# Kernel optimization log

Hardware: AMD Instinct MI355X
Metric: run time of the kernel (lower is better)

Reference implementation:

```python
import jax, jax.numpy as jnp
import numpy as np

PI = 3.141592653589793
M = 1500.0; IZ = 2250.0; LF = 1.2; LR = 1.6; CF = 80000.0; CR = 80000.0
TAU_A = 0.1; TAU_DELTA = 0.1
MAX_STEER = 30.0 * PI / 180.0
MAX_ACCEL = 3.0; MIN_ACCEL = -6.0
MU = 0.9; G = 9.81
L = LF + LR
FY_F_MAX = MU * M * G * (LR / L)
FY_R_MAX = MU * M * G * (LF / L)
V_EFF_MIN = 20.0 / 3.6
DT = 0.1
DT_INT = 0.01
B = 4194304


def setup_inputs() -> dict:
    key = jax.random.key(0)
    k1, k2 = jax.random.split(key)
    init_state = jax.random.normal(k1, (B, 9), dtype=jnp.float32)
    action = jax.random.normal(k2, (B, 2), dtype=jnp.float32)
    return {"init_state": init_state, "action": action}


def _substep(state, a_ref, h):
    # state: (B, 9) = [x, y, psi, v, a, delta, beta, r, delta_ref]
    x, y, psi, v, a, delta, beta, r, delta_ref = (state[:, i] for i in range(9))
    a_dot = (a_ref - a) / TAU_A
    delta_dot = (delta_ref - delta) / TAU_DELTA
    v_eff = jnp.maximum(v, V_EFF_MIN)
    alpha_f = beta + LF * r / v_eff - delta
    alpha_r = beta - LR * r / v_eff
    F_yf = jnp.clip(-CF * alpha_f, -FY_F_MAX, FY_F_MAX)
    F_yr = jnp.clip(-CR * alpha_r, -FY_R_MAX, FY_R_MAX)
    beta_dot = (F_yf + F_yr) / (M * v_eff) - r
    r_dot = (LF * F_yf - LR * F_yr) / IZ
    psi_eff = psi + beta
    new_state = jnp.stack([
        x + v * jnp.cos(psi_eff) * h,
        y + v * jnp.sin(psi_eff) * h,
        psi + r * h,
        jnp.maximum(v + a * h, 0.0),
        a + a_dot * h,
        jnp.clip(delta + delta_dot * h, -MAX_STEER, MAX_STEER),
        beta + beta_dot * h,
        r + r_dot * h,
        delta_ref,
    ], axis=1)
    return new_state


def _forward(init_state, action):
    # reset(): postprocess clamps
    s = init_state
    s = s.at[:, 3].set(jnp.maximum(s[:, 3], 0.0))
    s = s.at[:, 5].set(jnp.clip(s[:, 5], -MAX_STEER, MAX_STEER))
    s = s.at[:, 8].set(jnp.clip(s[:, 8], -MAX_STEER, MAX_STEER))
    # step(): ZOH action, clamp, overwrite delta_ref
    a_ref = jnp.clip(action[:, 0], MIN_ACCEL, MAX_ACCEL)
    delta_ref_cmd = jnp.clip(action[:, 1], -MAX_STEER, MAX_STEER)
    s = s.at[:, 8].set(delta_ref_cmd)
    # replicate torch's Python float substep bookkeeping exactly
    n_full = int(DT // DT_INT)
    dt_rem = DT - n_full * DT_INT
    h = jnp.float32(DT_INT)

    def body(st, _):
        return _substep(st, a_ref, h), None

    s, _ = jax.lax.scan(body, s, None, length=n_full)
    if dt_rem > 1e-12:
        s = _substep(s, a_ref, jnp.float32(dt_rem))
    return s


def reference(init_state, action):
    return _forward(init_state, action)
```

## Files before the change

### kernel.cpp

```cpp
#include <hip/hip_runtime.h>
#include <math.h>


__device__ __forceinline__ float med3(float x, float lo, float hi) {
    return __builtin_amdgcn_fmed3f(x, lo, hi);
}

__global__ __launch_bounds__(256) void bicycle_kernel(
    const float* __restrict__ state_in,
    const float* __restrict__ action_in,
    float* __restrict__ out)
{
    constexpr float MAX_STEER = (float)(30.0 * 3.141592653589793 / 180.0);
    constexpr float V_EFF_MIN = (float)(20.0 / 3.6);
    constexpr float FY_F_MAX  = (float)(0.9 * 1500.0 * 9.81 * (1.6 / 2.8));
    constexpr float FY_R_MAX  = (float)(0.9 * 1500.0 * 9.81 * (1.2 / 2.8));

    constexpr int RPB = 512;
    __shared__ float smem[RPB * 9];

    const int tid = threadIdx.x;
    const size_t rowBase = (size_t)blockIdx.x * RPB;

    const float4* g4 = (const float4*)(state_in + rowBase * 9);
    float4* l4 = (float4*)smem;
    l4[tid]        = g4[tid];
    l4[tid + 256]  = g4[tid + 256];
    l4[tid + 512]  = g4[tid + 512];
    l4[tid + 768]  = g4[tid + 768];
    if (tid < 128) l4[tid + 1024] = g4[tid + 1024];

    const float2* a2 = (const float2*)action_in + rowBase;
    float2 act[2];
    act[0] = a2[tid];
    act[1] = a2[tid + 256];
    __syncthreads();

    float x[2], y[2], psi[2], v[2], a[2], delta[2], beta[2], r[2];
    float a_ref[2], d_ref[2];

#pragma unroll
    for (int j = 0; j < 2; ++j) {
        const int rb = (tid + j * 256) * 9;
        x[j]     = smem[rb + 0];
        y[j]     = smem[rb + 1];
        psi[j]   = smem[rb + 2];
        v[j]     = fmaxf(smem[rb + 3], 0.0f);
        a[j]     = smem[rb + 4];
        delta[j] = med3(smem[rb + 5], -MAX_STEER, MAX_STEER);
        beta[j]  = smem[rb + 6];
        r[j]     = smem[rb + 7];
        a_ref[j] = med3(act[j].x, -6.0f, 3.0f);
        d_ref[j] = med3(act[j].y, -MAX_STEER, MAX_STEER);
    }

#pragma unroll
    for (int k = 0; k < 10; ++k) {
#pragma unroll
        for (int j = 0; j < 2; ++j) {
            float v_eff = fmaxf(v[j], V_EFF_MIN);
            float inv_v = __builtin_amdgcn_rcpf(v_eff);
            float t     = r[j] * inv_v;
            float alpha_f = fmaf(1.2f, t, beta[j]) - delta[j];
            float alpha_r = fmaf(-1.6f, t, beta[j]);
            float F_yf = med3(-80000.0f * alpha_f, -FY_F_MAX, FY_F_MAX);
            float F_yr = med3(-80000.0f * alpha_r, -FY_R_MAX, FY_R_MAX);
            float beta_dot = fmaf(F_yf + F_yr, inv_v * (1.0f / 1500.0f), -r[j]);
            float r_dot    = fmaf(1.2f, F_yf, -1.6f * F_yr) * (1.0f / 2250.0f);
            float sn, cs;
            __sincosf(psi[j] + beta[j], &sn, &cs);
            float vh = v[j] * 0.01f;
            x[j] = fmaf(vh, cs, x[j]);
            y[j] = fmaf(vh, sn, y[j]);
            float v_new = fmaxf(fmaf(a[j], 0.01f, v[j]), 0.0f);
            psi[j]   = fmaf(r[j], 0.01f, psi[j]);
            a[j]     = fmaf(a_ref[j] - a[j], 0.1f, a[j]);
            delta[j] = med3(fmaf(d_ref[j] - delta[j], 0.1f, delta[j]), -MAX_STEER, MAX_STEER);
            beta[j]  = fmaf(beta_dot, 0.01f, beta[j]);
            r[j]     = fmaf(r_dot, 0.01f, r[j]);
            v[j]     = v_new;
        }
    }

#pragma unroll
    for (int j = 0; j < 2; ++j) {
        const int rb = (tid + j * 256) * 9;
        smem[rb + 0] = x[j];
        smem[rb + 1] = y[j];
        smem[rb + 2] = psi[j];
        smem[rb + 3] = v[j];
        smem[rb + 4] = a[j];
        smem[rb + 5] = delta[j];
        smem[rb + 6] = beta[j];
        smem[rb + 7] = r[j];
        smem[rb + 8] = d_ref[j];
    }
    __syncthreads();

    float4* o4 = (float4*)(out + rowBase * 9);
    o4[tid]       = l4[tid];
    o4[tid + 256] = l4[tid + 256];
    o4[tid + 512] = l4[tid + 512];
    o4[tid + 768] = l4[tid + 768];
    if (tid < 128) o4[tid + 1024] = l4[tid + 1024];
}

extern "C" void kernel_launch(void* const* d_in, const int* in_sizes, int n_in,
                              void* d_out, int out_size, void* d_ws, size_t ws_size,
                              hipStream_t stream) {
    const float* state  = (const float*)d_in[0];
    const float* action = (const float*)d_in[1];
    float* out = (float*)d_out;
    const int rows = in_sizes[0] / 9;
    const int grid = rows / 512;
    bicycle_kernel<<<grid, 256, 0, stream>>>(state, action, out);
}
```

Baseline: 67.50 us.

## Pack two rows into float2 vectors and rotate sin/cos incrementally

Holds the two rows each thread handles in 2-wide vector types so the compiler can emit packed FP32 FMA/mul instructions. It also replaces the per-substep sincos with one initial sincos followed by a second-order angle-addition rotation driven by the heading increment (r + beta_dot)*h. The goal is fewer transcendental and scalar ALU ops in a kernel that is mostly memory bound. The rotation approximation adds a small error that grows over the substeps compared with computing sin/cos of psi+beta directly.

```diff
diff --git a/kernel.cpp b/kernel.cpp
--- a/kernel.cpp
+++ b/kernel.cpp
@@ -2,8 +2,13 @@
 #include <math.h>
 
 
+typedef float v2f __attribute__((ext_vector_type(2)));
+
 __device__ __forceinline__ float med3(float x, float lo, float hi) {
     return __builtin_amdgcn_fmed3f(x, lo, hi);
+}
+__device__ __forceinline__ v2f vfma(v2f a, v2f b, v2f c) {
+    return __builtin_elementwise_fma(a, b, c);
 }
 
 __global__ __launch_bounds__(256) void bicycle_kernel(
@@ -31,70 +36,79 @@
     if (tid < 128) l4[tid + 1024] = g4[tid + 1024];
 
     const float2* a2 = (const float2*)action_in + rowBase;
-    float2 act[2];
-    act[0] = a2[tid];
-    act[1] = a2[tid + 256];
+    float2 act0 = a2[tid];
+    float2 act1 = a2[tid + 256];
     __syncthreads();
 
-    float x[2], y[2], psi[2], v[2], a[2], delta[2], beta[2], r[2];
-    float a_ref[2], d_ref[2];
+    const int rb0 = tid * 9;
+    const int rb1 = (tid + 256) * 9;
+    v2f x, y, psi, v, a, delta, beta, r;
+    x     = (v2f){smem[rb0 + 0], smem[rb1 + 0]};
+    y     = (v2f){smem[rb0 + 1], smem[rb1 + 1]};
+    psi   = (v2f){smem[rb0 + 2], smem[rb1 + 2]};
+    v     = (v2f){fmaxf(smem[rb0 + 3], 0.0f), fmaxf(smem[rb1 + 3], 0.0f)};
+    a     = (v2f){smem[rb0 + 4], smem[rb1 + 4]};
+    delta = (v2f){med3(smem[rb0 + 5], -MAX_STEER, MAX_STEER),
+                  med3(smem[rb1 + 5], -MAX_STEER, MAX_STEER)};
+    beta  = (v2f){smem[rb0 + 6], smem[rb1 + 6]};
+    r     = (v2f){smem[rb0 + 7], smem[rb1 + 7]};
+    v2f a_ref = (v2f){med3(act0.x, -6.0f, 3.0f), med3(act1.x, -6.0f, 3.0f)};
+    v2f d_ref = (v2f){med3(act0.y, -MAX_STEER, MAX_STEER), med3(act1.y, -MAX_STEER, MAX_STEER)};
 
-#pragma unroll
-    for (int j = 0; j < 2; ++j) {
-        const int rb = (tid + j * 256) * 9;
-        x[j]     = smem[rb + 0];
-        y[j]     = smem[rb + 1];
-        psi[j]   = smem[rb + 2];
-        v[j]     = fmaxf(smem[rb + 3], 0.0f);
-        a[j]     = smem[rb + 4];
-        delta[j] = med3(smem[rb + 5], -MAX_STEER, MAX_STEER);
-        beta[j]  = smem[rb + 6];
-        r[j]     = smem[rb + 7];
-        a_ref[j] = med3(act[j].x, -6.0f, 3.0f);
-        d_ref[j] = med3(act[j].y, -MAX_STEER, MAX_STEER);
+    v2f cs, sn;
+    {
+        float s0, c0, s1, c1;
+        __sincosf(psi.x + beta.x, &s0, &c0);
+        __sincosf(psi.y + beta.y, &s1, &c1);
+        cs = (v2f){c0, c1};
+        sn = (v2f){s0, s1};
     }
 
 #pragma unroll
     for (int k = 0; k < 10; ++k) {
-#pragma unroll
-        for (int j = 0; j < 2; ++j) {
-            float v_eff = fmaxf(v[j], V_EFF_MIN);
-            float inv_v = __builtin_amdgcn_rcpf(v_eff);
-            float t     = r[j] * inv_v;
-            float alpha_f = fmaf(1.2f, t, beta[j]) - delta[j];
-            float alpha_r = fmaf(-1.6f, t, beta[j]);
-            float F_yf = med3(-80000.0f * alpha_f, -FY_F_MAX, FY_F_MAX);
-            float F_yr = med3(-80000.0f * alpha_r, -FY_R_MAX, FY_R_MAX);
-            float beta_dot = fmaf(F_yf + F_yr, inv_v * (1.0f / 1500.0f), -r[j]);
-            float r_dot    = fmaf(1.2f, F_yf, -1.6f * F_yr) * (1.0f / 2250.0f);
-            float sn, cs;
-            __sincosf(psi[j] + beta[j], &sn, &cs);
-            float vh = v[j] * 0.01f;
-            x[j] = fmaf(vh, cs, x[j]);
-            y[j] = fmaf(vh, sn, y[j]);
-            float v_new = fmaxf(fmaf(a[j], 0.01f, v[j]), 0.0f);
-            psi[j]   = fmaf(r[j], 0.01f, psi[j]);
-            a[j]     = fmaf(a_ref[j] - a[j], 0.1f, a[j]);
-            delta[j] = med3(fmaf(d_ref[j] - delta[j], 0.1f, delta[j]), -MAX_STEER, MAX_STEER);
-            beta[j]  = fmaf(beta_dot, 0.01f, beta[j]);
-            r[j]     = fmaf(r_dot, 0.01f, r[j]);
-            v[j]     = v_new;
-        }
+        v2f v_eff = {fmaxf(v.x, V_EFF_MIN), fmaxf(v.y, V_EFF_MIN)};
+        v2f inv_v = {__builtin_amdgcn_rcpf(v_eff.x), __builtin_amdgcn_rcpf(v_eff.y)};
+        v2f t = r * inv_v;
+        v2f alpha_f = vfma((v2f)(1.2f), t, beta) - delta;
+        v2f alpha_r = vfma((v2f)(-1.6f), t, beta);
+        v2f Ff_raw = alpha_f * -80000.0f;
+        v2f Fr_raw = alpha_r * -80000.0f;
+        v2f F_yf = {med3(Ff_raw.x, -FY_F_MAX, FY_F_MAX), med3(Ff_raw.y, -FY_F_MAX, FY_F_MAX)};
+        v2f F_yr = {med3(Fr_raw.x, -FY_R_MAX, FY_R_MAX), med3(Fr_raw.y, -FY_R_MAX, FY_R_MAX)};
+        v2f beta_dot = vfma(F_yf + F_yr, inv_v * (1.0f / 1500.0f), -r);
+        v2f r_dot = vfma((v2f)(1.2f), F_yf, F_yr * -1.6f) * (1.0f / 2250.0f);
+
+        v2f vh = v * 0.01f;
+        x = vfma(vh, cs, x);
+        y = vfma(vh, sn, y);
+
+        v2f d  = (r + beta_dot) * 0.01f;
+        v2f cd = vfma(d * d, (v2f)(-0.5f), (v2f)(1.0f));
+        v2f cs_n = vfma(cs, cd, -(sn * d));
+        v2f sn_n = vfma(sn, cd, cs * d);
+
+        v2f v_new = vfma(a, (v2f)(0.01f), v);
+        v_new = (v2f){fmaxf(v_new.x, 0.0f), fmaxf(v_new.y, 0.0f)};
+        psi  = vfma(r, (v2f)(0.01f), psi);
+        a    = vfma(a_ref - a, (v2f)(0.1f), a);
+        v2f dlt = vfma(d_ref - delta, (v2f)(0.1f), delta);
+        delta = (v2f){med3(dlt.x, -MAX_STEER, MAX_STEER), med3(dlt.y, -MAX_STEER, MAX_STEER)};
+        beta = vfma(beta_dot, (v2f)(0.01f), beta);
+        r    = vfma(r_dot, (v2f)(0.01f), r);
+        v = v_new;
+        cs = cs_n;
+        sn = sn_n;
     }
 
-#pragma unroll
-    for (int j = 0; j < 2; ++j) {
-        const int rb = (tid + j * 256) * 9;
-        smem[rb + 0] = x[j];
-        smem[rb + 1] = y[j];
-        smem[rb + 2] = psi[j];
-        smem[rb + 3] = v[j];
-        smem[rb + 4] = a[j];
-        smem[rb + 5] = delta[j];
-        smem[rb + 6] = beta[j];
-        smem[rb + 7] = r[j];
-        smem[rb + 8] = d_ref[j];
-    }
+    smem[rb0 + 0] = x.x;     smem[rb1 + 0] = x.y;
+    smem[rb0 + 1] = y.x;     smem[rb1 + 1] = y.y;
+    smem[rb0 + 2] = psi.x;   smem[rb1 + 2] = psi.y;
+    smem[rb0 + 3] = v.x;     smem[rb1 + 3] = v.y;
+    smem[rb0 + 4] = a.x;     smem[rb1 + 4] = a.y;
+    smem[rb0 + 5] = delta.x; smem[rb1 + 5] = delta.y;
+    smem[rb0 + 6] = beta.x;  smem[rb1 + 6] = beta.y;
+    smem[rb0 + 7] = r.x;     smem[rb1 + 7] = r.y;
+    smem[rb0 + 8] = d_ref.x; smem[rb1 + 8] = d_ref.y;
     __syncthreads();
 
     float4* o4 = (float4*)(out + rowBase * 9);
```

Measured after the change: 67.90 us. Within noise of the previous version (+0.6%).
